# Kernel tuning notes

Hardware: AMD Instinct MI355X
Metric: run time of the kernel (lower is better)

Reference implementation:

```python
import jax, jax.numpy as jnp
import numpy as np

B, T, H, C = 1024, 187, 256, 5


def setup_inputs() -> dict:
    key = jax.random.key(0)
    ks = jax.random.split(key, 11)
    s = 1.0 / np.sqrt(H)  # torch nn.RNN init scale
    return {
        "x": jax.random.normal(ks[0], (B, T), dtype=jnp.float32),
        "W_ih0": jax.random.uniform(ks[1], (H, 1), jnp.float32, -s, s),
        "W_hh0": jax.random.uniform(ks[2], (H, H), jnp.float32, -s, s),
        "b_ih0": jax.random.uniform(ks[3], (H,), jnp.float32, -s, s),
        "b_hh0": jax.random.uniform(ks[4], (H,), jnp.float32, -s, s),
        "W_ih1": jax.random.uniform(ks[5], (H, H), jnp.float32, -s, s),
        "W_hh1": jax.random.uniform(ks[6], (H, H), jnp.float32, -s, s),
        "b_ih1": jax.random.uniform(ks[7], (H,), jnp.float32, -s, s),
        "b_hh1": jax.random.uniform(ks[8], (H,), jnp.float32, -s, s),
        "W_fc": jax.random.uniform(ks[9], (C, H), jnp.float32, -s, s),
        "b_fc": jax.random.uniform(ks[10], (C,), jnp.float32, -s, s),
    }


def _rnn_layer(xp, W_hh):
    # xp: [T, B, H] precomputed input projection (incl. both biases)
    # h_t = tanh(xp_t + h_{t-1} @ W_hh^T)
    h0 = jnp.zeros(xp.shape[1:], dtype=xp.dtype)

    def step(h, xp_t):
        h_new = jnp.tanh(xp_t + h @ W_hh.T)
        return h_new, h_new

    _, hs = jax.lax.scan(step, h0, xp)
    return hs  # [T, B, H]


def reference(x, W_ih0, W_hh0, b_ih0, b_hh0, W_ih1, W_hh1, b_ih1, b_hh1, W_fc, b_fc):
    # x: [B, T] -> unsqueeze(-1) -> [B, T, 1]; input_size == 1
    # Layer 0 input projection: x * W_ih0[:,0] broadcast over H
    xp0 = x.T[:, :, None] * W_ih0[:, 0][None, None, :] + (b_ih0 + b_hh0)  # [T,B,H]
    hs0 = _rnn_layer(xp0, W_hh0)  # [T,B,H]
    # Layer 1 input projection
    xp1 = jnp.einsum("tbh,gh->tbg", hs0, W_ih1) + (b_ih1 + b_hh1)  # [T,B,H]
    hs1 = _rnn_layer(xp1, W_hh1)  # [T,B,H]
    last = hs1[-1]  # [B, H] == out[:, -1, :]
    # dropout p=0.0 (eval) is identity
    return last @ W_fc.T + b_fc  # [B, C]
```

## Files before the change

kernel.cpp:

```cpp
#include <hip/hip_runtime.h>
#include <stdint.h>


#define Bsz 1024
#define Tt  187
#define Hh  256
#define Cc  5
#define ST  264
#define XS  188

typedef _Float16 f16x8 __attribute__((ext_vector_type(8)));
typedef __fp16   fp16x2 __attribute__((ext_vector_type(2)));
typedef float    f32x4 __attribute__((ext_vector_type(4)));

__device__ __forceinline__ float tanh_fast(float z) {
    float e = __expf(2.0f * z);
    return 1.0f - 2.0f * __builtin_amdgcn_rcpf(1.0f + e);
}

__device__ __forceinline__ unsigned pk2(float a, float b) {
    union { fp16x2 h; unsigned u; } v;
    v.h = __builtin_amdgcn_cvt_pkrtz(a, b);
    return v.u;
}

__global__ __launch_bounds__(512, 1)
void rnn_fused(const float* __restrict__ x,
               const float* __restrict__ Wih0,
               const float* __restrict__ Whh0,
               const float* __restrict__ bih0,
               const float* __restrict__ bhh0,
               const float* __restrict__ Wih1,
               const float* __restrict__ Whh1,
               const float* __restrict__ bih1,
               const float* __restrict__ bhh1,
               const float* __restrict__ Wfc,
               const float* __restrict__ bfc,
               float* __restrict__ out)
{
    __shared__ __align__(16) _Float16 ht0[2][16 * ST];
    __shared__ __align__(16) _Float16 ht1[2][16 * ST];
    __shared__ float xs[16 * XS];

    const int tid  = threadIdx.x;
    const int lane = tid & 63;
    const int w    = tid >> 6;
    const int q    = lane >> 4;
    const int c    = lane & 15;
    const int bb   = blockIdx.x * 16;

    f16x8 wh0[2][8], wi1[2][8], wh1[2][8];
    f32x4 b0v[2], b1v[2], wi0v[2];
#pragma unroll
    for (int mt = 0; mt < 2; ++mt) {
        const int fb = 32 * w + 16 * mt;
#pragma unroll
        for (int r = 0; r < 4; ++r) {
            const int f = fb + 4 * q + r;
            b0v[mt][r]  = bih0[f] + bhh0[f];
            b1v[mt][r]  = bih1[f] + bhh1[f];
            wi0v[mt][r] = Wih0[f];
        }
        const int m = fb + c;
#pragma unroll
        for (int kt = 0; kt < 8; ++kt) {
            const int off = m * Hh + kt * 32 + q * 8;
            {
                const float4 a0 = *(const float4*)(Whh0 + off);
                const float4 a1 = *(const float4*)(Whh0 + off + 4);
                wh0[mt][kt] = (f16x8){(_Float16)a0.x, (_Float16)a0.y, (_Float16)a0.z, (_Float16)a0.w,
                                      (_Float16)a1.x, (_Float16)a1.y, (_Float16)a1.z, (_Float16)a1.w};
            }
            {
                const float4 a0 = *(const float4*)(Wih1 + off);
                const float4 a1 = *(const float4*)(Wih1 + off + 4);
                wi1[mt][kt] = (f16x8){(_Float16)a0.x, (_Float16)a0.y, (_Float16)a0.z, (_Float16)a0.w,
                                      (_Float16)a1.x, (_Float16)a1.y, (_Float16)a1.z, (_Float16)a1.w};
            }
            {
                const float4 a0 = *(const float4*)(Whh1 + off);
                const float4 a1 = *(const float4*)(Whh1 + off + 4);
                wh1[mt][kt] = (f16x8){(_Float16)a0.x, (_Float16)a0.y, (_Float16)a0.z, (_Float16)a0.w,
                                      (_Float16)a1.x, (_Float16)a1.y, (_Float16)a1.z, (_Float16)a1.w};
            }
        }
    }

    for (int i = tid; i < 16 * Tt; i += 512) {
        const int b = i / Tt, t = i - b * Tt;
        xs[b * XS + t] = x[(bb + b) * Tt + t];
    }
    {
        _Float16* z = &ht1[0][0];
        for (int i = tid; i < 2 * 16 * ST; i += 512) z[i] = (_Float16)0.f;
    }
    for (int i = tid; i < 16 * Hh; i += 512) {
        const int b = i >> 8, f = i & 255;
        const float xv0 = x[(bb + b) * Tt];
        ht0[0][b * ST + f] =
            (_Float16)tanh_fast(xv0 * Wih0[f] + bih0[f] + bhh0[f]);
    }
    __syncthreads();

    const int rdoff = c * ST + q * 8;
    const int wroff = c * ST + 32 * w + 4 * q;

#pragma unroll 1
    for (int s = 0; s < Tt; ++s) {
        const int cur = s & 1, nxt = cur ^ 1;
        const _Float16* B0p = &ht0[cur][rdoff];
        const _Float16* B1p = &ht1[nxt][rdoff];
        int sn = s + 1; if (sn >= Tt) sn = Tt - 1;
        const float xv = xs[c * XS + sn];

        f32x4 ai[2], ah0[2];
        {
            const f16x8 B = *(const f16x8*)B0p;
            ai[0]  = __builtin_amdgcn_mfma_f32_16x16x32_f16(wi1[0][0], B, b1v[0], 0, 0, 0);
            ai[1]  = __builtin_amdgcn_mfma_f32_16x16x32_f16(wi1[1][0], B, b1v[1], 0, 0, 0);
            ah0[0] = __builtin_amdgcn_mfma_f32_16x16x32_f16(wh0[0][0], B, b0v[0], 0, 0, 0);
            ah0[1] = __builtin_amdgcn_mfma_f32_16x16x32_f16(wh0[1][0], B, b0v[1], 0, 0, 0);
        }
#pragma unroll
        for (int kt = 1; kt < 8; ++kt) {
            const f16x8 B = *(const f16x8*)(B0p + kt * 32);
            ai[0]  = __builtin_amdgcn_mfma_f32_16x16x32_f16(wi1[0][kt], B, ai[0],  0, 0, 0);
            ai[1]  = __builtin_amdgcn_mfma_f32_16x16x32_f16(wi1[1][kt], B, ai[1],  0, 0, 0);
            ah0[0] = __builtin_amdgcn_mfma_f32_16x16x32_f16(wh0[0][kt], B, ah0[0], 0, 0, 0);
            ah0[1] = __builtin_amdgcn_mfma_f32_16x16x32_f16(wh0[1][kt], B, ah0[1], 0, 0, 0);
        }
#pragma unroll
        for (int mt = 0; mt < 2; ++mt) {
            const float t0 = tanh_fast(ah0[mt][0] + xv * wi0v[mt][0]);
            const float t1 = tanh_fast(ah0[mt][1] + xv * wi0v[mt][1]);
            const float t2 = tanh_fast(ah0[mt][2] + xv * wi0v[mt][2]);
            const float t3 = tanh_fast(ah0[mt][3] + xv * wi0v[mt][3]);
            *(uint2*)(&ht0[nxt][wroff + 16 * mt]) = make_uint2(pk2(t0, t1), pk2(t2, t3));
        }

        f32x4 ah1[2];
        {
            const f16x8 B = *(const f16x8*)B1p;
            const f32x4 z4 = (f32x4){0.f, 0.f, 0.f, 0.f};
            ah1[0] = __builtin_amdgcn_mfma_f32_16x16x32_f16(wh1[0][0], B, z4, 0, 0, 0);
            ah1[1] = __builtin_amdgcn_mfma_f32_16x16x32_f16(wh1[1][0], B, z4, 0, 0, 0);
        }
#pragma unroll
        for (int kt = 1; kt < 8; ++kt) {
            const f16x8 B = *(const f16x8*)(B1p + kt * 32);
            ah1[0] = __builtin_amdgcn_mfma_f32_16x16x32_f16(wh1[0][kt], B, ah1[0], 0, 0, 0);
            ah1[1] = __builtin_amdgcn_mfma_f32_16x16x32_f16(wh1[1][kt], B, ah1[1], 0, 0, 0);
        }
#pragma unroll
        for (int mt = 0; mt < 2; ++mt) {
            const float t0 = tanh_fast(ai[mt][0] + ah1[mt][0]);
            const float t1 = tanh_fast(ai[mt][1] + ah1[mt][1]);
            const float t2 = tanh_fast(ai[mt][2] + ah1[mt][2]);
            const float t3 = tanh_fast(ai[mt][3] + ah1[mt][3]);
            *(uint2*)(&ht1[cur][wroff + 16 * mt]) = make_uint2(pk2(t0, t1), pk2(t2, t3));
        }
        __syncthreads();
    }

    if (tid < 16 * Cc) {
        const int b = tid / Cc, cls = tid - Cc * (tid / Cc);
        const _Float16* h = &ht1[(Tt - 1) & 1][b * ST];
        float acc = bfc[cls];
        for (int k = 0; k < Hh; ++k)
            acc += (float)h[k] * Wfc[cls * Hh + k];
        out[(bb + b) * Cc + cls] = acc;
    }
}

extern "C" void kernel_launch(void* const* d_in, const int* in_sizes, int n_in,
                              void* d_out, int out_size, void* d_ws, size_t ws_size,
                              hipStream_t stream) {
    rnn_fused<<<dim3(Bsz / 16), dim3(512), 0, stream>>>(
        (const float*)d_in[0],
        (const float*)d_in[1],
        (const float*)d_in[2],
        (const float*)d_in[3],
        (const float*)d_in[4],
        (const float*)d_in[5],
        (const float*)d_in[6],
        (const float*)d_in[7],
        (const float*)d_in[8],
        (const float*)d_in[9],
        (const float*)d_in[10],
        (float*)d_out);
}
```

Measured before the change: 374.8 us.

## Halve block to four waves, each owning 64 features, spill weights to AGPRs/LDS

```diff
diff --git a/kernel.cpp b/kernel.cpp
--- a/kernel.cpp
+++ b/kernel.cpp
@@ -17,14 +17,19 @@
     float e = __expf(2.0f * z);
     return 1.0f - 2.0f * __builtin_amdgcn_rcpf(1.0f + e);
 }
-
 __device__ __forceinline__ unsigned pk2(float a, float b) {
     union { fp16x2 h; unsigned u; } v;
     v.h = __builtin_amdgcn_cvt_pkrtz(a, b);
     return v.u;
 }
+__device__ __forceinline__ f16x8 ld_frag(const float* p) {
+    const float4 a0 = *(const float4*)p;
+    const float4 a1 = *(const float4*)(p + 4);
+    return (f16x8){(_Float16)a0.x, (_Float16)a0.y, (_Float16)a0.z, (_Float16)a0.w,
+                   (_Float16)a1.x, (_Float16)a1.y, (_Float16)a1.z, (_Float16)a1.w};
+}
 
-__global__ __launch_bounds__(512, 1)
+__global__ __launch_bounds__(256, 1)
 void rnn_fused(const float* __restrict__ x,
                const float* __restrict__ Wih0,
                const float* __restrict__ Whh0,
@@ -41,6 +46,7 @@
     __shared__ __align__(16) _Float16 ht0[2][16 * ST];
     __shared__ __align__(16) _Float16 ht1[2][16 * ST];
     __shared__ float xs[16 * XS];
+    __shared__ f16x8 w1lds[4][4][2][64];
 
     const int tid  = threadIdx.x;
     const int lane = tid & 63;
@@ -49,11 +55,11 @@
     const int c    = lane & 15;
     const int bb   = blockIdx.x * 16;
 
-    f16x8 wh0[2][8], wi1[2][8], wh1[2][8];
-    f32x4 b0v[2], b1v[2], wi0v[2];
+    f16x8 wh0[4][8], wi1[4][8], wh1r[4][6];
+    f32x4 b0v[4], b1v[4], wi0v[4];
 #pragma unroll
-    for (int mt = 0; mt < 2; ++mt) {
-        const int fb = 32 * w + 16 * mt;
+    for (int mt = 0; mt < 4; ++mt) {
+        const int fb = 64 * w + 16 * mt;
 #pragma unroll
         for (int r = 0; r < 4; ++r) {
             const int f = fb + 4 * q + r;
@@ -65,36 +71,27 @@
 #pragma unroll
         for (int kt = 0; kt < 8; ++kt) {
             const int off = m * Hh + kt * 32 + q * 8;
-            {
-                const float4 a0 = *(const float4*)(Whh0 + off);
-                const float4 a1 = *(const float4*)(Whh0 + off + 4);
-                wh0[mt][kt] = (f16x8){(_Float16)a0.x, (_Float16)a0.y, (_Float16)a0.z, (_Float16)a0.w,
-                                      (_Float16)a1.x, (_Float16)a1.y, (_Float16)a1.z, (_Float16)a1.w};
-            }
-            {
-                const float4 a0 = *(const float4*)(Wih1 + off);
-                const float4 a1 = *(const float4*)(Wih1 + off + 4);
-                wi1[mt][kt] = (f16x8){(_Float16)a0.x, (_Float16)a0.y, (_Float16)a0.z, (_Float16)a0.w,
-                                      (_Float16)a1.x, (_Float16)a1.y, (_Float16)a1.z, (_Float16)a1.w};
-            }
-            {
-                const float4 a0 = *(const float4*)(Whh1 + off);
-                const float4 a1 = *(const float4*)(Whh1 + off + 4);
-                wh1[mt][kt] = (f16x8){(_Float16)a0.x, (_Float16)a0.y, (_Float16)a0.z, (_Float16)a0.w,
-                                      (_Float16)a1.x, (_Float16)a1.y, (_Float16)a1.z, (_Float16)a1.w};
-            }
+            wh0[mt][kt] = ld_frag(Whh0 + off);
+            wi1[mt][kt] = ld_frag(Wih1 + off);
+            f16x8 f = ld_frag(Whh1 + off);
+            if (kt < 6) wh1r[mt][kt] = f;
+            else        w1lds[w][mt][kt - 6][lane] = f;
         }
+        asm volatile("" : "+a"(wh0[mt][0]), "+a"(wh0[mt][1]), "+a"(wh0[mt][2]), "+a"(wh0[mt][3]),
+                          "+a"(wh0[mt][4]), "+a"(wh0[mt][5]), "+a"(wh0[mt][6]), "+a"(wh0[mt][7]),
+                          "+a"(wi1[mt][0]), "+a"(wi1[mt][1]), "+a"(wi1[mt][2]), "+a"(wi1[mt][3]),
+                          "+a"(wi1[mt][4]), "+a"(wi1[mt][5]), "+a"(wi1[mt][6]), "+a"(wi1[mt][7]));
     }
 
-    for (int i = tid; i < 16 * Tt; i += 512) {
+    for (int i = tid; i < 16 * Tt; i += 256) {
         const int b = i / Tt, t = i - b * Tt;
         xs[b * XS + t] = x[(bb + b) * Tt + t];
     }
     {
         _Float16* z = &ht1[0][0];
-        for (int i = tid; i < 2 * 16 * ST; i += 512) z[i] = (_Float16)0.f;
+        for (int i = tid; i < 2 * 16 * ST; i += 256) z[i] = (_Float16)0.f;
     }
-    for (int i = tid; i < 16 * Hh; i += 512) {
+    for (int i = tid; i < 16 * Hh; i += 256) {
         const int b = i >> 8, f = i & 255;
         const float xv0 = x[(bb + b) * Tt];
         ht0[0][b * ST + f] =
@@ -103,7 +100,7 @@
     __syncthreads();
 
     const int rdoff = c * ST + q * 8;
-    const int wroff = c * ST + 32 * w + 4 * q;
+    const int wroff = c * ST + 64 * w + 4 * q;
 
 #pragma unroll 1
     for (int s = 0; s < Tt; ++s) {
@@ -113,24 +110,20 @@
         int sn = s + 1; if (sn >= Tt) sn = Tt - 1;
         const float xv = xs[c * XS + sn];
 
-        f32x4 ai[2], ah0[2];
-        {
-            const f16x8 B = *(const f16x8*)B0p;
-            ai[0]  = __builtin_amdgcn_mfma_f32_16x16x32_f16(wi1[0][0], B, b1v[0], 0, 0, 0);
-            ai[1]  = __builtin_amdgcn_mfma_f32_16x16x32_f16(wi1[1][0], B, b1v[1], 0, 0, 0);
-            ah0[0] = __builtin_amdgcn_mfma_f32_16x16x32_f16(wh0[0][0], B, b0v[0], 0, 0, 0);
-            ah0[1] = __builtin_amdgcn_mfma_f32_16x16x32_f16(wh0[1][0], B, b0v[1], 0, 0, 0);
+        f32x4 ai[4], ah0[4];
+#pragma unroll
+        for (int mt = 0; mt < 4; ++mt) { ai[mt] = b1v[mt]; ah0[mt] = b0v[mt]; }
+#pragma unroll
+        for (int kt = 0; kt < 8; ++kt) {
+            const f16x8 B = *(const f16x8*)(B0p + kt * 32);
+#pragma unroll
+            for (int mt = 0; mt < 4; ++mt) {
+                ai[mt]  = __builtin_amdgcn_mfma_f32_16x16x32_f16(wi1[mt][kt], B, ai[mt],  0, 0, 0);
+                ah0[mt] = __builtin_amdgcn_mfma_f32_16x16x32_f16(wh0[mt][kt], B, ah0[mt], 0, 0, 0);
+            }
         }
 #pragma unroll
-        for (int kt = 1; kt < 8; ++kt) {
-            const f16x8 B = *(const f16x8*)(B0p + kt * 32);
-            ai[0]  = __builtin_amdgcn_mfma_f32_16x16x32_f16(wi1[0][kt], B, ai[0],  0, 0, 0);
-            ai[1]  = __builtin_amdgcn_mfma_f32_16x16x32_f16(wi1[1][kt], B, ai[1],  0, 0, 0);
-            ah0[0] = __builtin_amdgcn_mfma_f32_16x16x32_f16(wh0[0][kt], B, ah0[0], 0, 0, 0);
-            ah0[1] = __builtin_amdgcn_mfma_f32_16x16x32_f16(wh0[1][kt], B, ah0[1], 0, 0, 0);
-        }
-#pragma unroll
-        for (int mt = 0; mt < 2; ++mt) {
+        for (int mt = 0; mt < 4; ++mt) {
             const float t0 = tanh_fast(ah0[mt][0] + xv * wi0v[mt][0]);
             const float t1 = tanh_fast(ah0[mt][1] + xv * wi0v[mt][1]);
             const float t2 = tanh_fast(ah0[mt][2] + xv * wi0v[mt][2]);
@@ -138,21 +131,27 @@
             *(uint2*)(&ht0[nxt][wroff + 16 * mt]) = make_uint2(pk2(t0, t1), pk2(t2, t3));
         }
 
-        f32x4 ah1[2];
-        {
-            const f16x8 B = *(const f16x8*)B1p;
-            const f32x4 z4 = (f32x4){0.f, 0.f, 0.f, 0.f};
-            ah1[0] = __builtin_amdgcn_mfma_f32_16x16x32_f16(wh1[0][0], B, z4, 0, 0, 0);
-            ah1[1] = __builtin_amdgcn_mfma_f32_16x16x32_f16(wh1[1][0], B, z4, 0, 0, 0);
+        f32x4 ah1[4];
+#pragma unroll
+        for (int mt = 0; mt < 4; ++mt) ah1[mt] = (f32x4){0.f, 0.f, 0.f, 0.f};
+#pragma unroll
+        for (int kt = 0; kt < 6; ++kt) {
+            const f16x8 B = *(const f16x8*)(B1p + kt * 32);
+#pragma unroll
+            for (int mt = 0; mt < 4; ++mt)
+                ah1[mt] = __builtin_amdgcn_mfma_f32_16x16x32_f16(wh1r[mt][kt], B, ah1[mt], 0, 0, 0);
         }
 #pragma unroll
-        for (int kt = 1; kt < 8; ++kt) {
+        for (int kt = 6; kt < 8; ++kt) {
             const f16x8 B = *(const f16x8*)(B1p + kt * 32);
-            ah1[0] = __builtin_amdgcn_mfma_f32_16x16x32_f16(wh1[0][kt], B, ah1[0], 0, 0, 0);
-            ah1[1] = __builtin_amdgcn_mfma_f32_16x16x32_f16(wh1[1][kt], B, ah1[1], 0, 0, 0);
+#pragma unroll
+            for (int mt = 0; mt < 4; ++mt) {
+                const f16x8 A = w1lds[w][mt][kt - 6][lane];
+                ah1[mt] = __builtin_amdgcn_mfma_f32_16x16x32_f16(A, B, ah1[mt], 0, 0, 0);
+            }
         }
 #pragma unroll
-        for (int mt = 0; mt < 2; ++mt) {
+        for (int mt = 0; mt < 4; ++mt) {
             const float t0 = tanh_fast(ai[mt][0] + ah1[mt][0]);
             const float t1 = tanh_fast(ai[mt][1] + ah1[mt][1]);
             const float t2 = tanh_fast(ai[mt][2] + ah1[mt][2]);
@@ -175,7 +174,7 @@
 extern "C" void kernel_launch(void* const* d_in, const int* in_sizes, int n_in,
                               void* d_out, int out_size, void* d_ws, size_t ws_size,
                               hipStream_t stream) {
-    rnn_fused<<<dim3(Bsz / 16), dim3(512), 0, stream>>>(
+    rnn_fused<<<dim3(Bsz / 16), dim3(256), 0, stream>>>(
         (const float*)d_in[0],
         (const float*)d_in[1],
         (const float*)d_in[2],
```

New measurement: 458.7 us. 1.22x slower.
